# Kernel tuning notes

Measured on AMD Instinct MI355X. Metric: run time of the kernel, lower is better.

The kernel has to match this reference:

```python
import jax, jax.numpy as jnp
import numpy as np

EPS = 1e-5
SLOPE = 0.1


def _leaky(v):
    return jnp.where(v >= 0, v, SLOPE * v)


def _bn(v, gamma, beta):
    # v: (C, Q, k); training-mode batch norm over (Q, k) with biased variance
    m = v.mean(axis=(1, 2), keepdims=True)
    var = v.var(axis=(1, 2), keepdims=True)
    return (v - m) * jax.lax.rsqrt(var + EPS) * gamma[:, None, None] + beta[:, None, None]


def setup_inputs() -> dict:
    key = jax.random.key(0)
    ks = jax.random.split(key, 6)
    Q, S, K, F, O = 16384, 16384, 32, 64, 64
    q_points = jax.random.normal(ks[0], (Q, 3), dtype=jnp.float32)
    s_points = jax.random.normal(ks[1], (S, 3), dtype=jnp.float32)
    neighb_inds = jax.random.randint(ks[2], (Q, K), 0, S + 1)  # S is the padded zero row
    feat = jax.random.normal(ks[3], (S, F), dtype=jnp.float32)
    conv0_w = jax.random.normal(ks[4], (O, F), dtype=jnp.float32) * 0.1
    conv1_w = jax.random.normal(ks[5], (O * 3, O), dtype=jnp.float32) * 0.1
    return {
        "q_points": q_points,
        "s_points": s_points,
        "feat": feat,
        "neighb_inds": neighb_inds,
        "conv0_w": conv0_w,
        "gamma0": jnp.ones((O,), jnp.float32),
        "beta0": jnp.zeros((O,), jnp.float32),
        "conv1_w": conv1_w,
        "gamma1": jnp.ones((O,), jnp.float32),
        "beta1": jnp.zeros((O,), jnp.float32),
    }


def reference(q_points, s_points, feat, neighb_inds, conv0_w, gamma0, beta0, conv1_w, gamma1, beta1):
    Q, K = neighb_inds.shape
    n_supports = s_points.shape[0]
    out_c = conv1_w.shape[1]
    in_c = conv1_w.shape[0] // out_c  # = 3 for feat_mode='xyz'

    # pad with a zero row (index n_supports is the 'out of range' shadow point)
    s_pad = jnp.concatenate([s_points, jnp.zeros((1, s_points.shape[1]), s_points.dtype)], 0)
    f_pad = jnp.concatenate([feat, jnp.zeros((1, feat.shape[1]), feat.dtype)], 0)

    # relative xyz feature; zero out shadow neighbors
    x = s_pad[neighb_inds] - q_points[:, None, :]          # (Q, K, 3)
    mask = (neighb_inds == n_supports)[..., None]
    x = jnp.where(mask, jnp.zeros((), x.dtype), x)

    y = f_pad[neighb_inds]                                  # (Q, K, F)

    # kernel generation: conv0 (1x1) -> BN -> LeakyReLU -> conv1 (1x1)
    h = jnp.einsum('of,qkf->oqk', conv0_w, y)               # (O, Q, K)
    h = _leaky(_bn(h, gamma0, beta0))
    ker = jnp.einsum('co,oqk->qkc', conv1_w, h)             # (Q, K, O*in_c)
    ker = ker.reshape(Q, K, out_c, in_c)                    # (Q, K, O, 3)

    # per-edge matmul against relative xyz, then BN -> LeakyReLU -> max over k
    z = jnp.einsum('qkoi,qki->oqk', ker, x)                 # (O, Q, K)
    z = _leaky(_bn(z, gamma1, beta1))
    z = z.max(axis=2)                                       # (O, Q)
    return z.T                                              # (Q, O)
```

## Files before the change

### kernel.cpp

```cpp
#include <hip/hip_runtime.h>
#include <hip/hip_bf16.h>

typedef __attribute__((ext_vector_type(8))) short bf16x8;
typedef __attribute__((ext_vector_type(4))) short bf16x4;
typedef __attribute__((ext_vector_type(4))) float f32x4;

constexpr int Q = 16384, S = 16384, KNN = 32, F = 64, O = 64;
constexpr int NEDGE = Q * KNN;
constexpr int QB = 8;
constexpr int EB = 256;
constexpr int GD = Q / QB;
constexpr int GH = 256;
constexpr int FP = 72;
constexpr float EPSV = 1e-5f;

constexpr size_t CNT_OFF   = 0;
constexpr size_t CTR_OFF   = 65536;
constexpr size_t P0_OFF    = 65600;
constexpr size_t ST0_OFF   = P0_OFF + (size_t)GH * 128 * 4;
constexpr size_t ZMIN_OFF  = ST0_OFF + 512;
constexpr size_t P1T_OFF   = ZMIN_OFF + (size_t)Q * O * 4;
constexpr size_t ST1_OFF   = P1T_OFF + (size_t)128 * GD * 4;
constexpr size_t W0F_OFF   = ST1_OFF + 512;
constexpr size_t W1F_OFF   = W0F_OFF + 8192;
constexpr size_t FEATB_OFF = W1F_OFF + 24576;

__device__ __forceinline__ short f2bf(float f) {
  __hip_bfloat16 h = __float2bfloat16(f);
  short r; __builtin_memcpy(&r, &h, 2); return r;
}

__global__ void k_prep_hist(const float* __restrict__ w0g, const float* __restrict__ w1g,
                            short* __restrict__ w0f, short* __restrict__ w1f,
                            const float* __restrict__ feat, short* __restrict__ featb,
                            const int* __restrict__ inds, int* __restrict__ cnt) {
  __shared__ int lh[S];
  const int bx = blockIdx.x, tt = threadIdx.x;
  if (bx < 8) {
    const int t = bx * 256 + tt;
    const int fa = t >> 6, ln = t & 63;
    const int l4 = ln >> 4, l15 = ln & 15;
    if (fa < 8) {
      const int mt = fa >> 1, kk = fa & 1;
      const int o = 16 * mt + l15, f = 32 * kk + 8 * l4;
      const float* src = w0g + o * 64 + f;
      bf16x8 pk;
#pragma unroll
      for (int j = 0; j < 8; ++j) pk[j] = f2bf(src[j]);
      *(bf16x8*)&w0f[t * 8] = pk;
    } else {
      const int fb = fa - 8;
      const int nt = fb >> 1, kk = fb & 1;
      const int i = nt >> 2, b = nt & 3;
      const int o = 16 * b + l15, op = 32 * kk + 8 * l4;
      const float* src = w1g + (o * 3 + i) * 64 + op;
      bf16x8 pk;
#pragma unroll
      for (int j = 0; j < 8; ++j) pk[j] = f2bf(src[j]);
      *(bf16x8*)&w1f[(fb * 64 + ln) * 8] = pk;
    }
  } else if (bx < 72) {
    const int base = (bx - 8) * 16384;
#pragma unroll
    for (int j = 0; j < 8; ++j) {
      const int i = base + j * 2048 + tt * 8;
      f32x4 a = *(const f32x4*)(feat + i);
      f32x4 b = *(const f32x4*)(feat + i + 4);
      bf16x8 pk;
      pk[0] = f2bf(a[0]); pk[1] = f2bf(a[1]); pk[2] = f2bf(a[2]); pk[3] = f2bf(a[3]);
      pk[4] = f2bf(b[0]); pk[5] = f2bf(b[1]); pk[6] = f2bf(b[2]); pk[7] = f2bf(b[3]);
      *(bf16x8*)(featb + i) = pk;
    }
  } else {
    for (int c = tt; c < S; c += 256) lh[c] = 0;
    __syncthreads();
    const int4* ip = (const int4*)inds;
    const int base = (bx - 72) * 2048;
#pragma unroll
    for (int j = 0; j < 8; ++j) {
      const int4 v = ip[base + j * 256 + tt];
      if (v.x < S) atomicAdd(&lh[v.x], 1);
      if (v.y < S) atomicAdd(&lh[v.y], 1);
      if (v.z < S) atomicAdd(&lh[v.z], 1);
      if (v.w < S) atomicAdd(&lh[v.w], 1);
    }
    __syncthreads();
    for (int c = tt; c < S; c += 256) {
      const int v = lh[c];
      if (v) atomicAdd(&cnt[c], v);
    }
  }
}

__global__ void k_hsq(const short* __restrict__ featb, const int* __restrict__ cnt,
                      const short* __restrict__ w0f, float* __restrict__ p0,
                      int* __restrict__ ctr, const float* __restrict__ g0,
                      const float* __restrict__ b0, float* __restrict__ st0) {
  __shared__ float sred[4][2][64];
  __shared__ int isLast;
  const int t = threadIdx.x, blk = blockIdx.x;
  const int wv = t >> 6, ln = t & 63, l4 = ln >> 4, l15 = ln & 15;

  const bf16x8* w0v = (const bf16x8*)w0f;
  bf16x8 w0a[8];
#pragma unroll
  for (int fa = 0; fa < 8; ++fa) w0a[fa] = w0v[fa * 64 + ln];

  const int s0 = blk * 64 + wv * 16;
  const float wc = (float)cnt[s0 + l15];
  const short* fb = featb + (size_t)(s0 + l15) * F + 8 * l4;
  const bf16x8 y0 = *(const bf16x8*)(fb);
  const bf16x8 y1 = *(const bf16x8*)(fb + 32);

  float hs[4][4], hq[4][4];
#pragma unroll
  for (int mt = 0; mt < 4; ++mt) {
    f32x4 acc = {0.f, 0.f, 0.f, 0.f};
    acc = __builtin_amdgcn_mfma_f32_16x16x32_bf16(w0a[2 * mt], y0, acc, 0, 0, 0);
    acc = __builtin_amdgcn_mfma_f32_16x16x32_bf16(w0a[2 * mt + 1], y1, acc, 0, 0, 0);
#pragma unroll
    for (int r = 0; r < 4; ++r) {
      const float h = acc[r];
      hs[mt][r] = wc * h;
      hq[mt][r] = wc * h * h;
    }
  }
#pragma unroll
  for (int mt = 0; mt < 4; ++mt)
#pragma unroll
    for (int r = 0; r < 4; ++r) {
      float s = hs[mt][r], q = hq[mt][r];
#pragma unroll
      for (int d = 1; d < 16; d <<= 1) { s += __shfl_xor(s, d); q += __shfl_xor(q, d); }
      hs[mt][r] = s; hq[mt][r] = q;
    }
  if (l15 == 0) {
#pragma unroll
    for (int mt = 0; mt < 4; ++mt)
#pragma unroll
      for (int r = 0; r < 4; ++r) {
        const int o = 16 * mt + 4 * l4 + r;
        sred[wv][0][o] = hs[mt][r];
        sred[wv][1][o] = hq[mt][r];
      }
  }
  __syncthreads();
  if (t < 128) {
    const int qq = t >> 6, o = t & 63;
    p0[(size_t)blk * 128 + t] =
        sred[0][qq][o] + sred[1][qq][o] + sred[2][qq][o] + sred[3][qq][o];
  }
  __syncthreads();
  __threadfence();
  if (t == 0) isLast = (atomicAdd(&ctr[0], 1) == GH - 1);
  __syncthreads();
  if (isLast) {
    __threadfence();
    if (t < O) {
      float s = 0.f, q = 0.f;
      for (int b = 0; b < GH; ++b) {
        s += p0[(size_t)b * 128 + t];
        q += p0[(size_t)b * 128 + 64 + t];
      }
      const float invN = 1.f / (float)NEDGE;
      const float mean = s * invN;
      const float var = q * invN - mean * mean;
      const float sc = g0[t] * rsqrtf(var + EPSV);
      st0[t] = sc;
      st0[O + t] = b0[t] - mean * sc;
    }
  }
}

__launch_bounds__(256, 3)
__global__ void k_main(const float* __restrict__ qpts, const float* __restrict__ spts,
                       const short* __restrict__ featb, const int* __restrict__ inds,
                       const short* __restrict__ w0f, const short* __restrict__ w1f,
                       const float* __restrict__ st0,
                       float* __restrict__ zmax, float* __restrict__ zmin,
                       float* __restrict__ p1t) {
  __shared__ __align__(16) short hbuf[EB * FP];
  __shared__ __align__(16) float xs[3 * EB];

  const int t = threadIdx.x, blk = blockIdx.x;
  const int wv = t >> 6, ln = t & 63, l4 = ln >> 4, l15 = ln & 15;
  const int ebase = blk * EB;

  {
    const int e = t;
    const int idx = inds[ebase + e];
    const int q = blk * QB + (e >> 5);
    float x0 = 0.f, x1 = 0.f, x2 = 0.f;
    if (idx < S) {
      x0 = spts[idx * 3 + 0] - qpts[q * 3 + 0];
      x1 = spts[idx * 3 + 1] - qpts[q * 3 + 1];
      x2 = spts[idx * 3 + 2] - qpts[q * 3 + 2];
    }
    xs[0 * EB + e] = x0; xs[1 * EB + e] = x1; xs[2 * EB + e] = x2;
  }

  const bf16x8* w0v = (const bf16x8*)w0f;
  bf16x8 w0a[8];
#pragma unroll
  for (int fa = 0; fa < 8; ++fa) w0a[fa] = w0v[fa * 64 + ln];

  int idxr[4];
#pragma unroll
  for (int nt = 0; nt < 4; ++nt) idxr[nt] = inds[ebase + wv * 64 + nt * 16 + l15];

  bf16x8 yv[4][2];
#pragma unroll
  for (int nt = 0; nt < 4; ++nt) {
    if (idxr[nt] < S) {
      const short* fb = featb + (size_t)idxr[nt] * F + 8 * l4;
      yv[nt][0] = *(const bf16x8*)(fb);
      yv[nt][1] = *(const bf16x8*)(fb + 32);
    } else {
#pragma unroll
      for (int j = 0; j < 8; ++j) { yv[nt][0][j] = 0; yv[nt][1][j] = 0; }
    }
  }

  float scr[4][4], shr[4][4];
#pragma unroll
  for (int mt = 0; mt < 4; ++mt)
#pragma unroll
    for (int r = 0; r < 4; ++r) {
      const int o = 16 * mt + 4 * l4 + r;
      scr[mt][r] = st0[o]; shr[mt][r] = st0[O + o];
    }

#pragma unroll
  for (int nt = 0; nt < 4; ++nt) {
    const int erow = wv * 64 + nt * 16 + l15;
#pragma unroll
    for (int mt = 0; mt < 4; ++mt) {
      f32x4 acc = {0.f, 0.f, 0.f, 0.f};
      acc = __builtin_amdgcn_mfma_f32_16x16x32_bf16(w0a[2 * mt], yv[nt][0], acc, 0, 0, 0);
      acc = __builtin_amdgcn_mfma_f32_16x16x32_bf16(w0a[2 * mt + 1], yv[nt][1], acc, 0, 0, 0);
      bf16x4 hv;
#pragma unroll
      for (int r = 0; r < 4; ++r) {
        float v = acc[r] * scr[mt][r] + shr[mt][r];
        v = fmaxf(v, 0.1f * v);
        hv[r] = f2bf(v);
      }
      *(bf16x4*)&hbuf[erow * FP + 16 * mt + 4 * l4] = hv;
    }
  }

  bf16x8 hA[4][2];
#pragma unroll
  for (int mt = 0; mt < 4; ++mt) {
    const int erow = wv * 64 + mt * 16 + l15;
    hA[mt][0] = *(const bf16x8*)&hbuf[erow * FP + 8 * l4];
    hA[mt][1] = *(const bf16x8*)&hbuf[erow * FP + 32 + 8 * l4];
  }

  const bf16x8* w1v = (const bf16x8*)w1f;
  float zmx[2][4], zmn[2][4], zs[4], zq[4];
#pragma unroll
  for (int j = 0; j < 4; ++j) {
    zs[j] = 0.f; zq[j] = 0.f;
    zmx[0][j] = -3.4e38f; zmx[1][j] = -3.4e38f;
    zmn[0][j] = 3.4e38f;  zmn[1][j] = 3.4e38f;
  }

#pragma unroll
  for (int b = 0; b < 4; ++b) {
    bf16x8 w1b[6];
#pragma unroll
    for (int i = 0; i < 3; ++i)
#pragma unroll
      for (int kk = 0; kk < 2; ++kk)
        w1b[i * 2 + kk] = w1v[(((i * 4 + b) * 2) + kk) * 64 + ln];
#pragma unroll
    for (int mt = 0; mt < 4; ++mt) {
      const int ex = wv * 64 + mt * 16 + 4 * l4;
      f32x4 z4 = {0.f, 0.f, 0.f, 0.f};
#pragma unroll
      for (int i = 0; i < 3; ++i) {
        f32x4 acc = {0.f, 0.f, 0.f, 0.f};
        acc = __builtin_amdgcn_mfma_f32_16x16x32_bf16(hA[mt][0], w1b[2 * i], acc, 0, 0, 0);
        acc = __builtin_amdgcn_mfma_f32_16x16x32_bf16(hA[mt][1], w1b[2 * i + 1], acc, 0, 0, 0);
        const f32x4 xv = *(const f32x4*)&xs[i * EB + ex];
#pragma unroll
        for (int r = 0; r < 4; ++r) z4[r] += acc[r] * xv[r];
      }
      const int qh = mt >> 1;
#pragma unroll
      for (int r = 0; r < 4; ++r) {
        const float v = z4[r];
        zmx[qh][b] = fmaxf(zmx[qh][b], v);
        zmn[qh][b] = fminf(zmn[qh][b], v);
        zs[b] += v; zq[b] += v * v;
      }
    }
  }

#pragma unroll
  for (int qh = 0; qh < 2; ++qh)
#pragma unroll
    for (int b = 0; b < 4; ++b) {
      float m = zmx[qh][b];
      m = fmaxf(m, __shfl_xor(m, 16)); m = fmaxf(m, __shfl_xor(m, 32));
      zmx[qh][b] = m;
      float n = zmn[qh][b];
      n = fminf(n, __shfl_xor(n, 16)); n = fminf(n, __shfl_xor(n, 32));
      zmn[qh][b] = n;
    }
#pragma unroll
  for (int b = 0; b < 4; ++b) {
    float s = zs[b];  s += __shfl_xor(s, 16);  s += __shfl_xor(s, 32);  zs[b] = s;
    float sq = zq[b]; sq += __shfl_xor(sq, 16); sq += __shfl_xor(sq, 32); zq[b] = sq;
  }

  if (l4 == 0) {
#pragma unroll
    for (int qh = 0; qh < 2; ++qh) {
      const int q = blk * QB + wv * 2 + qh;
#pragma unroll
      for (int b = 0; b < 4; ++b) {
        zmax[(size_t)q * O + 16 * b + l15] = zmx[qh][b];
        zmin[(size_t)q * O + 16 * b + l15] = zmn[qh][b];
      }
    }
  }

  __syncthreads();
  if (l4 == 0) {
#pragma unroll
    for (int b = 0; b < 4; ++b) {
      xs[wv * 128 + 16 * b + l15] = zs[b];
      xs[wv * 128 + 64 + 16 * b + l15] = zq[b];
    }
  }
  __syncthreads();
  if (t < 128)
    p1t[(size_t)t * GD + blk] = xs[t] + xs[128 + t] + xs[256 + t] + xs[384 + t];
}

__global__ void k_red1(const float* __restrict__ p1t, const float* __restrict__ g1,
                       const float* __restrict__ b1, float* __restrict__ st1) {
  __shared__ float rs[256], rq[256];
  const int o = blockIdx.x, t = threadIdx.x;
  const float* ps = p1t + (size_t)o * GD;
  const float* pq = p1t + (size_t)(64 + o) * GD;
  float s = 0.f, q = 0.f;
#pragma unroll
  for (int j = 0; j < GD / 256; ++j) {
    s += ps[j * 256 + t];
    q += pq[j * 256 + t];
  }
  rs[t] = s; rq[t] = q;
  __syncthreads();
  for (int off = 128; off > 0; off >>= 1) {
    if (t < off) { rs[t] += rs[t + off]; rq[t] += rq[t + off]; }
    __syncthreads();
  }
  if (t == 0) {
    const float invN = 1.f / (float)NEDGE;
    const float mean = rs[0] * invN;
    const float var = rq[0] * invN - mean * mean;
    const float sc = g1[o] * rsqrtf(var + EPSV);
    st1[o] = sc;
    st1[O + o] = b1[o] - mean * sc;
  }
}

__global__ void k_final(const float* __restrict__ st1, const float* __restrict__ zmin,
                        float* __restrict__ out) {
  const int i4 = blockIdx.x * blockDim.x + threadIdx.x;
  const int o0 = (i4 * 4) & 63;
  const f32x4 mx = *(const f32x4*)(out + (size_t)i4 * 4);
  const f32x4 mn = *(const f32x4*)(zmin + (size_t)i4 * 4);
  const f32x4 sc = *(const f32x4*)(st1 + o0);
  const f32x4 sh = *(const f32x4*)(st1 + O + o0);
  f32x4 r;
#pragma unroll
  for (int j = 0; j < 4; ++j) {
    const float base = (sc[j] >= 0.f) ? mx[j] : mn[j];
    const float v = base * sc[j] + sh[j];
    r[j] = fmaxf(v, 0.1f * v);
  }
  *(f32x4*)(out + (size_t)i4 * 4) = r;
}

extern "C" void kernel_launch(void* const* d_in, const int* in_sizes, int n_in,
                              void* d_out, int out_size, void* d_ws, size_t ws_size,
                              hipStream_t stream) {
  const float* qpts = (const float*)d_in[0];
  const float* spts = (const float*)d_in[1];
  const float* feat = (const float*)d_in[2];
  const int*   inds = (const int*)d_in[3];
  const float* w0   = (const float*)d_in[4];
  const float* g0   = (const float*)d_in[5];
  const float* b0   = (const float*)d_in[6];
  const float* w1   = (const float*)d_in[7];
  const float* g1   = (const float*)d_in[8];
  const float* b1   = (const float*)d_in[9];
  float* out = (float*)d_out;

  char* ws = (char*)d_ws;
  int*   cnt   = (int*)(ws + CNT_OFF);
  int*   ctr   = (int*)(ws + CTR_OFF);
  float* p0    = (float*)(ws + P0_OFF);
  float* st0   = (float*)(ws + ST0_OFF);
  float* zmin  = (float*)(ws + ZMIN_OFF);
  float* p1t   = (float*)(ws + P1T_OFF);
  float* st1   = (float*)(ws + ST1_OFF);
  short* w0f   = (short*)(ws + W0F_OFF);
  short* w1f   = (short*)(ws + W1F_OFF);
  short* featb = (short*)(ws + FEATB_OFF);

  hipMemsetAsync(ws, 0, CTR_OFF + 64, stream);
  k_prep_hist<<<136, 256, 0, stream>>>(w0, w1, w0f, w1f, feat, featb, inds, cnt);
  k_hsq<<<GH, 256, 0, stream>>>(featb, cnt, w0f, p0, ctr, g0, b0, st0);
  k_main<<<GD, 256, 0, stream>>>(qpts, spts, featb, inds, w0f, w1f, st0, out, zmin, p1t);
  k_red1<<<64, 256, 0, stream>>>(p1t, g1, b1, st1);
  k_final<<<(Q * O) / 1024, 256, 0, stream>>>(st1, zmin, out);
}
```

Measured before the change: 86.67 us.

## Keep conv0 output in registers by permuting w1 K-layout, drop LDS staging

```diff
diff --git a/kernel.cpp b/kernel.cpp
--- a/kernel.cpp
+++ b/kernel.cpp
@@ -2,7 +2,6 @@
 #include <hip/hip_bf16.h>
 
 typedef __attribute__((ext_vector_type(8))) short bf16x8;
-typedef __attribute__((ext_vector_type(4))) short bf16x4;
 typedef __attribute__((ext_vector_type(4))) float f32x4;
 
 constexpr int Q = 16384, S = 16384, KNN = 32, F = 64, O = 64;
@@ -11,7 +10,6 @@
 constexpr int EB = 256;
 constexpr int GD = Q / QB;
 constexpr int GH = 256;
-constexpr int FP = 72;
 constexpr float EPSV = 1e-5f;
 
 constexpr size_t CNT_OFF   = 0;
@@ -19,8 +17,8 @@
 constexpr size_t P0_OFF    = 65600;
 constexpr size_t ST0_OFF   = P0_OFF + (size_t)GH * 128 * 4;
 constexpr size_t ZMIN_OFF  = ST0_OFF + 512;
-constexpr size_t P1T_OFF   = ZMIN_OFF + (size_t)Q * O * 4;
-constexpr size_t ST1_OFF   = P1T_OFF + (size_t)128 * GD * 4;
+constexpr size_t P1_OFF    = ZMIN_OFF + (size_t)Q * O * 4;
+constexpr size_t ST1_OFF   = P1_OFF + (size_t)GD * 128 * 4;
 constexpr size_t W0F_OFF   = ST1_OFF + 512;
 constexpr size_t W1F_OFF   = W0F_OFF + 8192;
 constexpr size_t FEATB_OFF = W1F_OFF + 24576;
@@ -52,11 +50,14 @@
       const int fb = fa - 8;
       const int nt = fb >> 1, kk = fb & 1;
       const int i = nt >> 2, b = nt & 3;
-      const int o = 16 * b + l15, op = 32 * kk + 8 * l4;
-      const float* src = w1g + (o * 3 + i) * 64 + op;
+      const int o = 16 * b + l15;
+      const float* row = w1g + (o * 3 + i) * 64;
+      const int base = 32 * kk + 4 * l4;
       bf16x8 pk;
 #pragma unroll
-      for (int j = 0; j < 8; ++j) pk[j] = f2bf(src[j]);
+      for (int j = 0; j < 4; ++j) pk[j] = f2bf(row[base + j]);
+#pragma unroll
+      for (int j = 4; j < 8; ++j) pk[j] = f2bf(row[base + 16 + (j & 3)]);
       *(bf16x8*)&w1f[(fb * 64 + ln) * 8] = pk;
     }
   } else if (bx < 72) {
@@ -172,15 +173,15 @@
   }
 }
 
-__launch_bounds__(256, 3)
+__launch_bounds__(256, 4)
 __global__ void k_main(const float* __restrict__ qpts, const float* __restrict__ spts,
                        const short* __restrict__ featb, const int* __restrict__ inds,
                        const short* __restrict__ w0f, const short* __restrict__ w1f,
                        const float* __restrict__ st0,
                        float* __restrict__ zmax, float* __restrict__ zmin,
-                       float* __restrict__ p1t) {
-  __shared__ __align__(16) short hbuf[EB * FP];
+                       float* __restrict__ p1) {
   __shared__ __align__(16) float xs[3 * EB];
+  __shared__ float swred[512];
 
   const int t = threadIdx.x, blk = blockIdx.x;
   const int wv = t >> 6, ln = t & 63, l4 = ln >> 4, l15 = ln & 15;
@@ -208,53 +209,46 @@
 #pragma unroll
   for (int nt = 0; nt < 4; ++nt) idxr[nt] = inds[ebase + wv * 64 + nt * 16 + l15];
 
-  bf16x8 yv[4][2];
-#pragma unroll
-  for (int nt = 0; nt < 4; ++nt) {
-    if (idxr[nt] < S) {
-      const short* fb = featb + (size_t)idxr[nt] * F + 8 * l4;
-      yv[nt][0] = *(const bf16x8*)(fb);
-      yv[nt][1] = *(const bf16x8*)(fb + 32);
+  const float* scp = st0 + 4 * l4;
+  const float* shp = st0 + O + 4 * l4;
+  bf16x8 hA[4][2];
+#pragma unroll
+  for (int T = 0; T < 4; ++T) {
+    bf16x8 y0, y1;
+    if (idxr[T] < S) {
+      const short* fbp = featb + (size_t)idxr[T] * F + 8 * l4;
+      y0 = *(const bf16x8*)(fbp);
+      y1 = *(const bf16x8*)(fbp + 32);
     } else {
 #pragma unroll
-      for (int j = 0; j < 8; ++j) { yv[nt][0][j] = 0; yv[nt][1][j] = 0; }
-    }
-  }
-
-  float scr[4][4], shr[4][4];
-#pragma unroll
-  for (int mt = 0; mt < 4; ++mt)
-#pragma unroll
-    for (int r = 0; r < 4; ++r) {
-      const int o = 16 * mt + 4 * l4 + r;
-      scr[mt][r] = st0[o]; shr[mt][r] = st0[O + o];
-    }
-
-#pragma unroll
-  for (int nt = 0; nt < 4; ++nt) {
-    const int erow = wv * 64 + nt * 16 + l15;
-#pragma unroll
-    for (int mt = 0; mt < 4; ++mt) {
-      f32x4 acc = {0.f, 0.f, 0.f, 0.f};
-      acc = __builtin_amdgcn_mfma_f32_16x16x32_bf16(w0a[2 * mt], yv[nt][0], acc, 0, 0, 0);
-      acc = __builtin_amdgcn_mfma_f32_16x16x32_bf16(w0a[2 * mt + 1], yv[nt][1], acc, 0, 0, 0);
-      bf16x4 hv;
+      for (int j = 0; j < 8; ++j) { y0[j] = 0; y1[j] = 0; }
+    }
+#pragma unroll
+    for (int kk = 0; kk < 2; ++kk) {
+      f32x4 a0 = {0.f, 0.f, 0.f, 0.f}, a1 = {0.f, 0.f, 0.f, 0.f};
+      a0 = __builtin_amdgcn_mfma_f32_16x16x32_bf16(w0a[4 * kk + 0], y0, a0, 0, 0, 0);
+      a0 = __builtin_amdgcn_mfma_f32_16x16x32_bf16(w0a[4 * kk + 1], y1, a0, 0, 0, 0);
+      a1 = __builtin_amdgcn_mfma_f32_16x16x32_bf16(w0a[4 * kk + 2], y0, a1, 0, 0, 0);
+      a1 = __builtin_amdgcn_mfma_f32_16x16x32_bf16(w0a[4 * kk + 3], y1, a1, 0, 0, 0);
+      const f32x4 sc0 = *(const f32x4*)(scp + 32 * kk);
+      const f32x4 sh0 = *(const f32x4*)(shp + 32 * kk);
+      const f32x4 sc1 = *(const f32x4*)(scp + 32 * kk + 16);
+      const f32x4 sh1 = *(const f32x4*)(shp + 32 * kk + 16);
+      bf16x8 h;
 #pragma unroll
       for (int r = 0; r < 4; ++r) {
-        float v = acc[r] * scr[mt][r] + shr[mt][r];
+        float v = a0[r] * sc0[r] + sh0[r];
         v = fmaxf(v, 0.1f * v);
-        hv[r] = f2bf(v);
-      }
-      *(bf16x4*)&hbuf[erow * FP + 16 * mt + 4 * l4] = hv;
-    }
-  }
-
-  bf16x8 hA[4][2];
-#pragma unroll
-  for (int mt = 0; mt < 4; ++mt) {
-    const int erow = wv * 64 + mt * 16 + l15;
-    hA[mt][0] = *(const bf16x8*)&hbuf[erow * FP + 8 * l4];
-    hA[mt][1] = *(const bf16x8*)&hbuf[erow * FP + 32 + 8 * l4];
+        h[r] = f2bf(v);
+      }
+#pragma unroll
+      for (int r = 0; r < 4; ++r) {
+        float v = a1[r] * sc1[r] + sh1[r];
+        v = fmaxf(v, 0.1f * v);
+        h[4 + r] = f2bf(v);
+      }
+      hA[T][kk] = h;
+    }
   }
 
   const bf16x8* w1v = (const bf16x8*)w1f;
@@ -325,32 +319,25 @@
         zmin[(size_t)q * O + 16 * b + l15] = zmn[qh][b];
       }
     }
-  }
-
-  __syncthreads();
-  if (l4 == 0) {
 #pragma unroll
     for (int b = 0; b < 4; ++b) {
-      xs[wv * 128 + 16 * b + l15] = zs[b];
-      xs[wv * 128 + 64 + 16 * b + l15] = zq[b];
+      swred[wv * 128 + 16 * b + l15] = zs[b];
+      swred[wv * 128 + 64 + 16 * b + l15] = zq[b];
     }
   }
   __syncthreads();
   if (t < 128)
-    p1t[(size_t)t * GD + blk] = xs[t] + xs[128 + t] + xs[256 + t] + xs[384 + t];
-}
-
-__global__ void k_red1(const float* __restrict__ p1t, const float* __restrict__ g1,
+    p1[(size_t)blk * 128 + t] = swred[t] + swred[128 + t] + swred[256 + t] + swred[384 + t];
+}
+
+__global__ void k_red1(const float* __restrict__ p1, const float* __restrict__ g1,
                        const float* __restrict__ b1, float* __restrict__ st1) {
   __shared__ float rs[256], rq[256];
   const int o = blockIdx.x, t = threadIdx.x;
-  const float* ps = p1t + (size_t)o * GD;
-  const float* pq = p1t + (size_t)(64 + o) * GD;
   float s = 0.f, q = 0.f;
-#pragma unroll
-  for (int j = 0; j < GD / 256; ++j) {
-    s += ps[j * 256 + t];
-    q += pq[j * 256 + t];
+  for (int r = t; r < GD; r += 256) {
+    s += p1[(size_t)r * 128 + o];
+    q += p1[(size_t)r * 128 + 64 + o];
   }
   rs[t] = s; rq[t] = q;
   __syncthreads();
@@ -407,7 +394,7 @@
   float* p0    = (float*)(ws + P0_OFF);
   float* st0   = (float*)(ws + ST0_OFF);
   float* zmin  = (float*)(ws + ZMIN_OFF);
-  float* p1t   = (float*)(ws + P1T_OFF);
+  float* p1    = (float*)(ws + P1_OFF);
   float* st1   = (float*)(ws + ST1_OFF);
   short* w0f   = (short*)(ws + W0F_OFF);
   short* w1f   = (short*)(ws + W1F_OFF);
@@ -416,7 +403,7 @@
   hipMemsetAsync(ws, 0, CTR_OFF + 64, stream);
   k_prep_hist<<<136, 256, 0, stream>>>(w0, w1, w0f, w1f, feat, featb, inds, cnt);
   k_hsq<<<GH, 256, 0, stream>>>(featb, cnt, w0f, p0, ctr, g0, b0, st0);
-  k_main<<<GD, 256, 0, stream>>>(qpts, spts, featb, inds, w0f, w1f, st0, out, zmin, p1t);
-  k_red1<<<64, 256, 0, stream>>>(p1t, g1, b1, st1);
+  k_main<<<GD, 256, 0, stream>>>(qpts, spts, featb, inds, w0f, w1f, st0, out, zmin, p1);
+  k_red1<<<64, 256, 0, stream>>>(p1, g1, b1, st1);
   k_final<<<(Q * O) / 1024, 256, 0, stream>>>(st1, zmin, out);
 }
```

Measured after the change: 183.1 us. 2.11x slower.
